# Optimization experiments

Hardware: AMD Instinct MI355X
Metric: run time of the kernel (lower is better)

The kernel has to match this reference:

```python
import jax, jax.numpy as jnp
from jax import lax
import numpy as np

K_SIZE = 3  # SteerableKernelBase.create_radial(3)


def _radial_basis_3x3():
    """Orthonormal radial steerable basis on a 3x3 grid.
    Returns 6 unit-norm kernels: [k0_center, k0_ring, k1_cos, k1_sin, k2_cos, k2_sin]."""
    ys, xs = np.mgrid[-1:2, -1:2].astype(np.float32)
    ang = np.arctan2(ys, xs)
    ring = (np.hypot(xs, ys) > 0).astype(np.float32)

    def unit(k):
        return (k / np.linalg.norm(k)).astype(np.float32)

    b0c = np.zeros((3, 3), np.float32); b0c[1, 1] = 1.0
    basis = np.stack([
        b0c,                       # k=0, r=0
        unit(ring),                # k=0, r=1
        unit(np.cos(ang) * ring),  # k=1 real
        unit(np.sin(ang) * ring),  # k=1 imag
        unit(np.cos(2 * ang) * ring),  # k=2 real
        unit(np.sin(2 * ang) * ring),  # k=2 imag
    ])
    return jnp.asarray(basis)  # (6, 3, 3)


def setup_inputs() -> dict:
    key = jax.random.key(0)
    k1, k2, k3 = jax.random.split(key, 3)
    N, C_in, C_out, H, W = 16, 64, 64, 128, 128
    x = jax.random.normal(k1, (N, C_in, H, W), dtype=jnp.float32)
    # steering angle field in [0,1); alpha = (cos 2*pi*theta, sin 2*pi*theta) is unitary
    theta = jax.random.uniform(k2, (N, 1, H, W), dtype=jnp.float32)
    # steerable weights: (n_out, n_in, 4) -> [k0 center, k0 ring, k1, k2]
    fan_in = C_in * K_SIZE * K_SIZE
    std = jnp.sqrt(2.0 / fan_in)  # relu gain init as in steerable_base.init_weights
    weights = jax.random.normal(k3, (C_out, C_in, 4), dtype=jnp.float32) * std
    bias = jnp.zeros((C_out,), dtype=jnp.float32)
    return {"x": x, "theta": theta, "weights": weights, "bias": bias}


def reference(x, theta, weights, bias):
    basis = _radial_basis_3x3()  # (6,3,3)
    O = weights.shape[0]
    w = weights[..., None, None]  # (O,I,4,1,1)
    # Synthesize per-harmonic kernels (O,I,3,3) from the steerable basis
    k0 = w[:, :, 0] * basis[0] + w[:, :, 1] * basis[1]
    k1r = w[:, :, 2] * basis[2]
    k1i = w[:, :, 2] * basis[3]
    k2r = w[:, :, 3] * basis[4]
    k2i = w[:, :, 3] * basis[5]
    ker = jnp.concatenate([k0, k1r, k1i, k2r, k2i], axis=0)  # (5O, I, 3, 3)

    z = lax.conv_general_dilated(
        x, ker, window_strides=(1, 1), padding="SAME",
        dimension_numbers=("NCHW", "OIHW", "NCHW"))  # (N, 5O, H, W)
    N, _, H, W = z.shape
    z = z.reshape(N, 5, O, H, W)

    # angle harmonics cos(k*alpha), sin(k*alpha); alpha unitary so rho=1 path
    a = 2.0 * jnp.pi * theta  # (N,1,H,W)
    c1, s1 = jnp.cos(a), jnp.sin(a)
    c2 = 2.0 * c1 * c1 - 1.0
    s2 = 2.0 * s1 * c1

    out = (z[:, 0] + c1 * z[:, 1] + s1 * z[:, 2]
           + c2 * z[:, 3] + s2 * z[:, 4])
    return out + bias[None, :, None, None]
```

## Files before the change

kernel.cpp:

```cpp
#include <hip/hip_runtime.h>


typedef __bf16 bf16x8 __attribute__((ext_vector_type(8)));
typedef float  f32x16 __attribute__((ext_vector_type(16)));
typedef float  f32x4  __attribute__((ext_vector_type(4)));
typedef unsigned int u32;
typedef const __attribute__((address_space(1))) u32* gp_t;
typedef __attribute__((address_space(3))) u32* lp_t;

#define HH 128
#define WW 128
#define CHCH 8
#define NCHUNK 8
#define NBUF 3
#define RROWS 10
#define RCOLS 40
#define CHF 400
#define CHIMG 65536

__global__ void wt_repack(const float* __restrict__ wt,
                          unsigned short* __restrict__ wb) {
    int i = blockIdx.x * 256 + threadIdx.x;
    int o = i >> 8, k = i & 255;
    union { float f; u32 u; } v; v.f = wt[i];
    unsigned short b = (unsigned short)((v.u + 0x7FFF + ((v.u >> 16) & 1)) >> 16);
    int kcg = k >> 4, hxx = (k >> 3) & 1, r = k & 7;
    wb[((kcg * 2 + hxx) * 64 + o) * 8 + r] = b;
}

__global__ __launch_bounds__(256, 4) void steered_conv_mfma(
    const float* __restrict__ x, const float* __restrict__ theta,
    const unsigned short* __restrict__ wb, const float* __restrict__ bias,
    float* __restrict__ out)
{
    __shared__ __attribute__((aligned(16))) float lds[NBUF][CHCH][CHF];

    const int tid = threadIdx.x;
    const int wid = tid >> 6, lane = tid & 63;
    const int pc = lane & 31, hx = lane >> 5;

    const int bb = blockIdx.x;
    const int swz = (bb & 7) * 128 + (bb >> 3);
    const int n = swz >> 6;
    const int ty = (swz >> 2) & 15, tx = swz & 3;
    const int h0 = ty * 8, w0 = tx * 32;
    const int p0 = wid * 2;

    const int oA = lane * 16;
    const int rA = oA / 160;
    const int cA = oA - rA * 160;
    int ghA = h0 - 1 + rA; ghA = ghA < 0 ? 0 : (ghA > 127 ? 127 : ghA);
    int srcA = ghA * 512 + w0 * 4 - 16 + cA;
    srcA = srcA < 0 ? 0 : srcA;
    const bool skA = (w0 == 0 && cA < 16) || (w0 == 96 && cA >= 144)
                   || (h0 == 0 && rA == 0);

    const int oB = 1024 + lane * 16;
    const int rB = oB / 160;
    const int cB = oB - rB * 160;
    int ghB = h0 - 1 + rB; ghB = ghB < 0 ? 0 : (ghB > 127 ? 127 : ghB);
    int srcB = ghB * 512 + w0 * 4 - 16 + cB;
    srcB = srcB < 0 ? 0 : (srcB > CHIMG - 16 ? CHIMG - 16 : srcB);
    const bool skB = (lane >= 36) || (w0 == 0 && cB < 16) || (w0 == 96 && cB >= 144)
                   || (h0 == 120 && rB == 9);

    const char* xn = (const char*)x + (size_t)n * 64 * CHIMG;

    float s1a, c1a, s1b, c1b;
    __sincosf(6.2831853071795864769f * theta[(n*HH + h0+p0)*WW + w0+pc], &s1a, &c1a);
    __sincosf(6.2831853071795864769f * theta[(n*HH + h0+p0+1)*WW + w0+pc], &s1b, &c1b);
    const float c2a = 2.f*c1a*c1a - 1.f, s2a = 2.f*s1a*c1a;
    const float c2b = 2.f*c1b*c1b - 1.f, s2b = 2.f*s1b*c1b;

    if ((h0 == 0) | (h0 == 120) | (w0 == 0) | (w0 == 96)) {
        f32x4* z = (f32x4*)&lds[0][0][0];
        for (int i = tid; i < NBUF * CHCH * CHF / 4; i += 256)
            z[i] = f32x4{0.f, 0.f, 0.f, 0.f};
    }
    __syncthreads();

    auto stage = [&](int t) {
        const char* xc = xn + (size_t)(t * CHCH) * CHIMG;
        #pragma unroll
        for (int j = 0; j < 2; ++j) {
            const int ch = wid * 2 + j;
            const char* s = xc + ch * CHIMG;
            char* d = (char*)&lds[t % NBUF][ch][0];
            if (!skA) __builtin_amdgcn_global_load_lds((gp_t)(s + srcA), (lp_t)d, 16, 0, 0);
            if (!skB) __builtin_amdgcn_global_load_lds((gp_t)(s + srcB), (lp_t)(d + 1024), 16, 0, 0);
        }
    };

    stage(0);
    stage(1);

    f32x16 acc00, acc01, acc10, acc11;
    #pragma unroll
    for (int r = 0; r < 16; ++r) { acc00[r]=0.f; acc01[r]=0.f; acc10[r]=0.f; acc11[r]=0.f; }

    const float RS  = 0.35355339059327373f;
    const float HMR = 0.14644660940672627f;
    const unsigned short* wbl = wb + (hx * 64 + pc) * 8;

    #pragma unroll
    for (int c = 0; c < NCHUNK; ++c) {
        asm volatile("s_waitcnt vmcnt(4)" ::: "memory");
        const unsigned short* wr0 = wbl + c * 2048;
        const bf16x8 A00 = *(const bf16x8*)(wr0);
        const bf16x8 A01 = *(const bf16x8*)(wr0 + 256);
        const bf16x8 A10 = *(const bf16x8*)(wr0 + 1024);
        const bf16x8 A11 = *(const bf16x8*)(wr0 + 1280);
        __builtin_amdgcn_sched_barrier(0);
        __builtin_amdgcn_s_barrier();
        if (c < NCHUNK - 2) stage(c + 2);
        __builtin_amdgcn_sched_barrier(0);

        const float* tb = &lds[c % NBUF][0][p0 * RCOLS + pc + 3];
        #pragma unroll
        for (int kc = 0; kc < 2; ++kc) {
            bf16x8 b0, b1;
            #pragma unroll
            for (int cs = 0; cs < 2; ++cs) {
                const float* t = tb + (kc * 4 + hx * 2 + cs) * CHF;
                const float t00=t[0],   t01=t[1],   t02=t[2];
                const float t10=t[40],  t11=t[41],  t12=t[42];
                const float t20=t[80],  t21=t[81],  t22=t[82];
                const float t30=t[120], t31=t[121], t32=t[122];
                const float S0=t00+t01+t02, S1=t10+t11+t12;
                const float S2=t20+t21+t22, S3=t30+t31+t32;
                const float D0=t02-t00, D1=t12-t10, D2=t22-t20, D3=t32-t30;
                {
                    const float F1 = RS * (S0 + S2 + S1 - t11);
                    const float B2 = RS * (D0 + D2) + 0.5f * D1;
                    const float B3 = RS * (S2 - S0) + HMR * (t21 - t01);
                    const float B4 = 0.5f * (S1 - t11 - t01 - t21);
                    const float B5 = 0.5f * (D2 - D0);
                    b0[cs*4+0] = (__bf16)t11;
                    b0[cs*4+1] = (__bf16)F1;
                    b0[cs*4+2] = (__bf16)(c1a * B2 + s1a * B3);
                    b0[cs*4+3] = (__bf16)(c2a * B4 + s2a * B5);
                }
                {
                    const float F1 = RS * (S1 + S3 + S2 - t21);
                    const float B2 = RS * (D1 + D3) + 0.5f * D2;
                    const float B3 = RS * (S3 - S1) + HMR * (t31 - t11);
                    const float B4 = 0.5f * (S2 - t21 - t11 - t31);
                    const float B5 = 0.5f * (D3 - D1);
                    b1[cs*4+0] = (__bf16)t21;
                    b1[cs*4+1] = (__bf16)F1;
                    b1[cs*4+2] = (__bf16)(c1b * B2 + s1b * B3);
                    b1[cs*4+3] = (__bf16)(c2b * B4 + s2b * B5);
                }
            }
            const bf16x8 A0 = kc ? A10 : A00;
            const bf16x8 A1 = kc ? A11 : A01;
            __builtin_amdgcn_s_setprio(1);
            acc00 = __builtin_amdgcn_mfma_f32_32x32x16_bf16(A0, b0, acc00, 0, 0, 0);
            acc01 = __builtin_amdgcn_mfma_f32_32x32x16_bf16(A1, b0, acc01, 0, 0, 0);
            acc10 = __builtin_amdgcn_mfma_f32_32x32x16_bf16(A0, b1, acc10, 0, 0, 0);
            acc11 = __builtin_amdgcn_mfma_f32_32x32x16_bf16(A1, b1, acc11, 0, 0, 0);
            __builtin_amdgcn_s_setprio(0);
        }
    }

    const size_t hw = (size_t)HH * WW;
    float* op = out + (size_t)n * 64 * hw + (size_t)(h0 + p0) * WW + w0 + pc;
    #pragma unroll
    for (int r = 0; r < 16; ++r) {
        const int o = (r & 3) + 8 * (r >> 2) + 4 * hx;
        const float bo = bias[o], bo2 = bias[o + 32];
        op[(size_t)o * hw]             = acc00[r] + bo;
        op[(size_t)(o + 32) * hw]      = acc01[r] + bo2;
        op[(size_t)o * hw + WW]        = acc10[r] + bo;
        op[(size_t)(o + 32) * hw + WW] = acc11[r] + bo2;
    }
}

extern "C" void kernel_launch(void* const* d_in, const int* in_sizes, int n_in,
                              void* d_out, int out_size, void* d_ws, size_t ws_size,
                              hipStream_t stream) {
    const float* x     = (const float*)d_in[0];
    const float* theta = (const float*)d_in[1];
    const float* wt    = (const float*)d_in[2];
    const float* bias  = (const float*)d_in[3];
    float* out = (float*)d_out;
    unsigned short* wb = (unsigned short*)d_ws;

    wt_repack<<<64, 256, 0, stream>>>(wt, wb);

    steered_conv_mfma<<<1024, 256, 0, stream>>>(x, theta, wb, bias, out);
}
```

Baseline: 41.91 us.

## Use full-width 1024-thread tiles with LDS-resident weights and double-buffered input rows

Blocks now cover a full 128-column, 8-row strip with 16 waves instead of a 32-column tile with 4 waves. This removes the horizontal halo duplication; left and right borders are handled by clamped indices and multiplication by 0/1 masks. The whole bf16 weight matrix is loaded once into LDS per block instead of being read from global memory each chunk. Input staging drops from triple to double buffering with a full vmcnt(0) wait every chunk, which may expose more load latency. The larger LDS footprint and 1024-thread blocks also cut occupancy, and only 256 blocks are launched.

```diff
diff --git a/kernel.cpp b/kernel.cpp
--- a/kernel.cpp
+++ b/kernel.cpp
@@ -3,19 +3,13 @@
 
 typedef __bf16 bf16x8 __attribute__((ext_vector_type(8)));
 typedef float  f32x16 __attribute__((ext_vector_type(16)));
-typedef float  f32x4  __attribute__((ext_vector_type(4)));
 typedef unsigned int u32;
 typedef const __attribute__((address_space(1))) u32* gp_t;
 typedef __attribute__((address_space(3))) u32* lp_t;
 
 #define HH 128
 #define WW 128
-#define CHCH 8
-#define NCHUNK 8
-#define NBUF 3
-#define RROWS 10
-#define RCOLS 40
-#define CHF 400
+#define HW 16384
 #define CHIMG 65536
 
 __global__ void wt_repack(const float* __restrict__ wt,
@@ -28,71 +22,84 @@
     wb[((kcg * 2 + hxx) * 64 + o) * 8 + r] = b;
 }
 
-__global__ __launch_bounds__(256, 4) void steered_conv_mfma(
+__global__ __launch_bounds__(1024, 4) void steered_conv_mfma(
     const float* __restrict__ x, const float* __restrict__ theta,
     const unsigned short* __restrict__ wb, const float* __restrict__ bias,
     float* __restrict__ out)
 {
-    __shared__ __attribute__((aligned(16))) float lds[NBUF][CHCH][CHF];
+    __shared__ unsigned short wlds[16384];
+    __shared__ __attribute__((aligned(16))) float xb[2][8][12][128];
 
-    const int tid = threadIdx.x;
-    const int wid = tid >> 6, lane = tid & 63;
-    const int pc = lane & 31, hx = lane >> 5;
+    const int tid  = threadIdx.x;
+    const int W    = tid >> 6, lane = tid & 63;
+    const int pc   = lane & 31, hx = lane >> 5;
+    const int p0   = (W >> 2) * 2;
+    const int w    = (W & 3) * 32 + pc;
 
-    const int bb = blockIdx.x;
-    const int swz = (bb & 7) * 128 + (bb >> 3);
-    const int n = swz >> 6;
-    const int ty = (swz >> 2) & 15, tx = swz & 3;
-    const int h0 = ty * 8, w0 = tx * 32;
-    const int p0 = wid * 2;
-
-    const int oA = lane * 16;
-    const int rA = oA / 160;
-    const int cA = oA - rA * 160;
-    int ghA = h0 - 1 + rA; ghA = ghA < 0 ? 0 : (ghA > 127 ? 127 : ghA);
-    int srcA = ghA * 512 + w0 * 4 - 16 + cA;
-    srcA = srcA < 0 ? 0 : srcA;
-    const bool skA = (w0 == 0 && cA < 16) || (w0 == 96 && cA >= 144)
-                   || (h0 == 0 && rA == 0);
-
-    const int oB = 1024 + lane * 16;
-    const int rB = oB / 160;
-    const int cB = oB - rB * 160;
-    int ghB = h0 - 1 + rB; ghB = ghB < 0 ? 0 : (ghB > 127 ? 127 : ghB);
-    int srcB = ghB * 512 + w0 * 4 - 16 + cB;
-    srcB = srcB < 0 ? 0 : (srcB > CHIMG - 16 ? CHIMG - 16 : srcB);
-    const bool skB = (lane >= 36) || (w0 == 0 && cB < 16) || (w0 == 96 && cB >= 144)
-                   || (h0 == 120 && rB == 9);
+    const int bb  = blockIdx.x;
+    const int swz = (bb & 7) * 32 + (bb >> 3);
+    const int n   = swz >> 4;
+    const int h0  = (swz & 15) * 8;
 
     const char* xn = (const char*)x + (size_t)n * 64 * CHIMG;
 
+    {
+        const char* s = (const char*)wb + tid * 16;
+        char* d = (char*)wlds + W * 1024;
+        __builtin_amdgcn_global_load_lds((gp_t)s, (lp_t)d, 16, 0, 0);
+        __builtin_amdgcn_global_load_lds((gp_t)(s + 16384), (lp_t)(d + 16384), 16, 0, 0);
+    }
+
+    const int i0  = W * 3;
+    const int ch0 = i0 / 6,       pr0 = i0 - ch0 * 6;
+    const int ch1 = (i0+1) / 6,   pr1 = (i0+1) - ch1 * 6;
+    const int ch2 = (i0+2) / 6,   pr2 = (i0+2) - ch2 * 6;
+    char* const xldsb = (char*)&xb[0][0][0][0];
+
+    auto stage = [&](int t) {
+        const char* xc = xn + (size_t)(t * 8) * CHIMG + lane * 16;
+        char* db = xldsb + (t & 1) * 49152;
+        if (!((h0 == 0 && pr0 == 0) || (h0 == 120 && pr0 == 5)))
+            __builtin_amdgcn_global_load_lds(
+                (gp_t)(xc + ch0 * CHIMG + (h0 - 2 + 2 * pr0) * 512),
+                (lp_t)(db + ch0 * 6144 + pr0 * 1024), 16, 0, 0);
+        if (!((h0 == 0 && pr1 == 0) || (h0 == 120 && pr1 == 5)))
+            __builtin_amdgcn_global_load_lds(
+                (gp_t)(xc + ch1 * CHIMG + (h0 - 2 + 2 * pr1) * 512),
+                (lp_t)(db + ch1 * 6144 + pr1 * 1024), 16, 0, 0);
+        if (!((h0 == 0 && pr2 == 0) || (h0 == 120 && pr2 == 5)))
+            __builtin_amdgcn_global_load_lds(
+                (gp_t)(xc + ch2 * CHIMG + (h0 - 2 + 2 * pr2) * 512),
+                (lp_t)(db + ch2 * 6144 + pr2 * 1024), 16, 0, 0);
+    };
+    stage(0);
+
     float s1a, c1a, s1b, c1b;
-    __sincosf(6.2831853071795864769f * theta[(n*HH + h0+p0)*WW + w0+pc], &s1a, &c1a);
-    __sincosf(6.2831853071795864769f * theta[(n*HH + h0+p0+1)*WW + w0+pc], &s1b, &c1b);
+    __sincosf(6.2831853071795864769f * theta[(n*HH + h0+p0)*WW + w], &s1a, &c1a);
+    __sincosf(6.2831853071795864769f * theta[(n*HH + h0+p0+1)*WW + w], &s1b, &c1b);
     const float c2a = 2.f*c1a*c1a - 1.f, s2a = 2.f*s1a*c1a;
     const float c2b = 2.f*c1b*c1b - 1.f, s2b = 2.f*s1b*c1b;
 
-    if ((h0 == 0) | (h0 == 120) | (w0 == 0) | (w0 == 96)) {
-        f32x4* z = (f32x4*)&lds[0][0][0];
-        for (int i = tid; i < NBUF * CHCH * CHF / 4; i += 256)
-            z[i] = f32x4{0.f, 0.f, 0.f, 0.f};
+    if (h0 == 0 || h0 == 120) {
+        const int sb = (h0 == 0) ? 0 : 10;
+        for (int i = tid; i < 4096; i += 1024) {
+            const int b   = i >> 11;
+            const int ch  = (i >> 8) & 7;
+            const int rr  = (i >> 7) & 1;
+            const int col = i & 127;
+            xb[b][ch][sb + rr][col] = 0.f;
+        }
     }
     __syncthreads();
 
-    auto stage = [&](int t) {
-        const char* xc = xn + (size_t)(t * CHCH) * CHIMG;
-        #pragma unroll
-        for (int j = 0; j < 2; ++j) {
-            const int ch = wid * 2 + j;
-            const char* s = xc + ch * CHIMG;
-            char* d = (char*)&lds[t % NBUF][ch][0];
-            if (!skA) __builtin_amdgcn_global_load_lds((gp_t)(s + srcA), (lp_t)d, 16, 0, 0);
-            if (!skB) __builtin_amdgcn_global_load_lds((gp_t)(s + srcB), (lp_t)(d + 1024), 16, 0, 0);
-        }
-    };
+    const float fL = (w > 0) ? 1.f : 0.f;
+    const float fR = (w < WW - 1) ? 1.f : 0.f;
+    const int  wLo = (w > 0) ? w - 1 : 0;
+    const int  wRo = (w < WW - 1) ? w + 1 : WW - 1;
 
-    stage(0);
-    stage(1);
+    const float* pL = &xb[0][0][0][0] + hx * 3072 + (p0 + 1) * 128 + wLo;
+    const float* pC = &xb[0][0][0][0] + hx * 3072 + (p0 + 1) * 128 + w;
+    const float* pR = &xb[0][0][0][0] + hx * 3072 + (p0 + 1) * 128 + wRo;
 
     f32x16 acc00, acc01, acc10, acc11;
     #pragma unroll
@@ -100,60 +107,60 @@
 
     const float RS  = 0.35355339059327373f;
     const float HMR = 0.14644660940672627f;
-    const unsigned short* wbl = wb + (hx * 64 + pc) * 8;
 
     #pragma unroll
-    for (int c = 0; c < NCHUNK; ++c) {
-        asm volatile("s_waitcnt vmcnt(4)" ::: "memory");
-        const unsigned short* wr0 = wbl + c * 2048;
-        const bf16x8 A00 = *(const bf16x8*)(wr0);
-        const bf16x8 A01 = *(const bf16x8*)(wr0 + 256);
-        const bf16x8 A10 = *(const bf16x8*)(wr0 + 1024);
-        const bf16x8 A11 = *(const bf16x8*)(wr0 + 1280);
+    for (int c = 0; c < 8; ++c) {
+        asm volatile("s_waitcnt vmcnt(0)" ::: "memory");
+        __builtin_amdgcn_s_barrier();
         __builtin_amdgcn_sched_barrier(0);
-        __builtin_amdgcn_s_barrier();
-        if (c < NCHUNK - 2) stage(c + 2);
+        if (c < 7) stage(c + 1);
         __builtin_amdgcn_sched_barrier(0);
 
-        const float* tb = &lds[c % NBUF][0][p0 * RCOLS + pc + 3];
         #pragma unroll
         for (int kc = 0; kc < 2; ++kc) {
+            const int kcg = c * 2 + kc;
+            const bf16x8 A0 = *(const bf16x8*)&wlds[((kcg*2 + hx)*64 + pc) * 8];
+            const bf16x8 A1 = *(const bf16x8*)&wlds[((kcg*2 + hx)*64 + 32 + pc) * 8];
             bf16x8 b0, b1;
             #pragma unroll
             for (int cs = 0; cs < 2; ++cs) {
-                const float* t = tb + (kc * 4 + hx * 2 + cs) * CHF;
-                const float t00=t[0],   t01=t[1],   t02=t[2];
-                const float t10=t[40],  t11=t[41],  t12=t[42];
-                const float t20=t[80],  t21=t[81],  t22=t[82];
-                const float t30=t[120], t31=t[121], t32=t[122];
-                const float S0=t00+t01+t02, S1=t10+t11+t12;
-                const float S2=t20+t21+t22, S3=t30+t31+t32;
-                const float D0=t02-t00, D1=t12-t10, D2=t22-t20, D3=t32-t30;
+                const int off = (c & 1) * 12288 + (kc * 4 + cs) * 1536;
+                float S[4], D[4], C[4];
+                #pragma unroll
+                for (int r = 0; r < 4; ++r) {
+                    const float tL = pL[off + r * 128];
+                    const float tC = pC[off + r * 128];
+                    const float tR = pR[off + r * 128];
+                    const float a = fL * tL, cc = fR * tR;
+                    S[r] = a + tC + cc;
+                    D[r] = cc - a;
+                    C[r] = tC;
+                }
                 {
-                    const float F1 = RS * (S0 + S2 + S1 - t11);
-                    const float B2 = RS * (D0 + D2) + 0.5f * D1;
-                    const float B3 = RS * (S2 - S0) + HMR * (t21 - t01);
-                    const float B4 = 0.5f * (S1 - t11 - t01 - t21);
-                    const float B5 = 0.5f * (D2 - D0);
-                    b0[cs*4+0] = (__bf16)t11;
+                    const float T  = S[1] - C[1];
+                    const float F1 = RS * (S[0] + S[2] + T);
+                    const float B2 = RS * (D[0] + D[2]) + 0.5f * D[1];
+                    const float B3 = RS * (S[2] - S[0]) + HMR * (C[2] - C[0]);
+                    const float B4 = 0.5f * (T - (C[0] + C[2]));
+                    const float B5 = 0.5f * (D[2] - D[0]);
+                    b0[cs*4+0] = (__bf16)C[1];
                     b0[cs*4+1] = (__bf16)F1;
                     b0[cs*4+2] = (__bf16)(c1a * B2 + s1a * B3);
                     b0[cs*4+3] = (__bf16)(c2a * B4 + s2a * B5);
                 }
                 {
-                    const float F1 = RS * (S1 + S3 + S2 - t21);
-                    const float B2 = RS * (D1 + D3) + 0.5f * D2;
-                    const float B3 = RS * (S3 - S1) + HMR * (t31 - t11);
-                    const float B4 = 0.5f * (S2 - t21 - t11 - t31);
-                    const float B5 = 0.5f * (D3 - D1);
-                    b1[cs*4+0] = (__bf16)t21;
+                    const float T  = S[2] - C[2];
+                    const float F1 = RS * (S[1] + S[3] + T);
+                    const float B2 = RS * (D[1] + D[3]) + 0.5f * D[2];
+                    const float B3 = RS * (S[3] - S[1]) + HMR * (C[3] - C[1]);
+                    const float B4 = 0.5f * (T - (C[1] + C[3]));
+                    const float B5 = 0.5f * (D[3] - D[1]);
+                    b1[cs*4+0] = (__bf16)C[2];
                     b1[cs*4+1] = (__bf16)F1;
                     b1[cs*4+2] = (__bf16)(c1b * B2 + s1b * B3);
                     b1[cs*4+3] = (__bf16)(c2b * B4 + s2b * B5);
                 }
             }
-            const bf16x8 A0 = kc ? A10 : A00;
-            const bf16x8 A1 = kc ? A11 : A01;
             __builtin_amdgcn_s_setprio(1);
             acc00 = __builtin_amdgcn_mfma_f32_32x32x16_bf16(A0, b0, acc00, 0, 0, 0);
             acc01 = __builtin_amdgcn_mfma_f32_32x32x16_bf16(A1, b0, acc01, 0, 0, 0);
@@ -163,8 +170,8 @@
         }
     }
 
-    const size_t hw = (size_t)HH * WW;
-    float* op = out + (size_t)n * 64 * hw + (size_t)(h0 + p0) * WW + w0 + pc;
+    const size_t hw = (size_t)HW;
+    float* op = out + (size_t)n * 64 * hw + (size_t)(h0 + p0) * WW + w;
     #pragma unroll
     for (int r = 0; r < 16; ++r) {
         const int o = (r & 3) + 8 * (r >> 2) + 4 * hx;
@@ -188,5 +195,5 @@
 
     wt_repack<<<64, 256, 0, stream>>>(wt, wb);
 
-    steered_conv_mfma<<<1024, 256, 0, stream>>>(x, theta, wb, bias, out);
+    steered_conv_mfma<<<256, 1024, 0, stream>>>(x, theta, wb, bias, out);
 }
```

Result: slower. 57.23 us (+36.5%).

## Prefetch weight fragments one chunk ahead with double-buffered registers

Applied to the files above, without the earlier changes.

Weight A-operand loads for the next channel chunk are issued a chunk early into alternating even/odd register sets, so the MFMA loop no longer waits on global weight loads issued at the top of the same iteration. The vmcnt accounting is adjusted to drain all loads on the last chunk. Launch bounds drop from 4 to 3 waves-per-EU occupancy hint to give room for the extra 32 VGPRs of prefetched weights. This trades occupancy for latency hiding; the vmcnt(4) count may now be inconsistent with the extra in-flight weight loads mixed with LDS DMA loads.

```diff
diff --git a/kernel.cpp b/kernel.cpp
--- a/kernel.cpp
+++ b/kernel.cpp
@@ -28,7 +28,7 @@
     wb[((kcg * 2 + hxx) * 64 + o) * 8 + r] = b;
 }
 
-__global__ __launch_bounds__(256, 4) void steered_conv_mfma(
+__global__ __launch_bounds__(256, 3) void steered_conv_mfma(
     const float* __restrict__ x, const float* __restrict__ theta,
     const unsigned short* __restrict__ wb, const float* __restrict__ bias,
     float* __restrict__ out)
@@ -91,7 +91,17 @@
         }
     };
 
+    const unsigned short* wbl = wb + (hx * 64 + pc) * 8;
+    bf16x8 wE0, wE1, wE2, wE3, wO0, wO1, wO2, wO3;
+
     stage(0);
+    {
+        const unsigned short* wr = wbl;
+        wE0 = *(const bf16x8*)(wr);
+        wE1 = *(const bf16x8*)(wr + 256);
+        wE2 = *(const bf16x8*)(wr + 1024);
+        wE3 = *(const bf16x8*)(wr + 1280);
+    }
     stage(1);
 
     f32x16 acc00, acc01, acc10, acc11;
@@ -100,20 +110,34 @@
 
     const float RS  = 0.35355339059327373f;
     const float HMR = 0.14644660940672627f;
-    const unsigned short* wbl = wb + (hx * 64 + pc) * 8;
 
     #pragma unroll
     for (int c = 0; c < NCHUNK; ++c) {
-        asm volatile("s_waitcnt vmcnt(4)" ::: "memory");
-        const unsigned short* wr0 = wbl + c * 2048;
-        const bf16x8 A00 = *(const bf16x8*)(wr0);
-        const bf16x8 A01 = *(const bf16x8*)(wr0 + 256);
-        const bf16x8 A10 = *(const bf16x8*)(wr0 + 1024);
-        const bf16x8 A11 = *(const bf16x8*)(wr0 + 1280);
+        if (c == NCHUNK - 1) asm volatile("s_waitcnt vmcnt(0)" ::: "memory");
+        else                 asm volatile("s_waitcnt vmcnt(4)" ::: "memory");
         __builtin_amdgcn_sched_barrier(0);
         __builtin_amdgcn_s_barrier();
-        if (c < NCHUNK - 2) stage(c + 2);
+        if (c + 1 < NCHUNK) {
+            const unsigned short* wr = wbl + (c + 1) * 2048;
+            if ((c + 1) & 1) {
+                wO0 = *(const bf16x8*)(wr);
+                wO1 = *(const bf16x8*)(wr + 256);
+                wO2 = *(const bf16x8*)(wr + 1024);
+                wO3 = *(const bf16x8*)(wr + 1280);
+            } else {
+                wE0 = *(const bf16x8*)(wr);
+                wE1 = *(const bf16x8*)(wr + 256);
+                wE2 = *(const bf16x8*)(wr + 1024);
+                wE3 = *(const bf16x8*)(wr + 1280);
+            }
+        }
+        if (c + 2 < NCHUNK) stage(c + 2);
         __builtin_amdgcn_sched_barrier(0);
+
+        const bf16x8 A00 = (c & 1) ? wO0 : wE0;
+        const bf16x8 A01 = (c & 1) ? wO1 : wE1;
+        const bf16x8 A10 = (c & 1) ? wO2 : wE2;
+        const bf16x8 A11 = (c & 1) ? wO3 : wE3;
 
         const float* tb = &lds[c % NBUF][0][p0 * RCOLS + pc + 3];
         #pragma unroll
```

Result: no change. 41.84 us (-0.2%).

## Use 512-thread blocks with one output row per wave and LDS-staged weights

Applied to the files above, without the earlier changes.

Doubles the block to 8 waves so each wave computes a single output row with two accumulators, where previously each wave did two rows with four. The repacked bf16 weights are staged once per block into LDS with async global-to-LDS loads, replacing per-chunk global loads. Each stage now has one wave per input channel, and explicit left/right edge masks are added to the 3x3 stencil math. The intent is more waves to hide latency and cheaper weight access. In exchange, each output row now reads and reduces its own three input rows, losing the row reuse the two-row scheme had, and LDS use grows to roughly 70 KB per block, which limits how many blocks fit per CU.

```diff
diff --git a/kernel.cpp b/kernel.cpp
--- a/kernel.cpp
+++ b/kernel.cpp
@@ -10,12 +10,9 @@
 
 #define HH 128
 #define WW 128
-#define CHCH 8
+#define HW 16384
 #define NCHUNK 8
 #define NBUF 3
-#define RROWS 10
-#define RCOLS 40
-#define CHF 400
 #define CHIMG 65536
 
 __global__ void wt_repack(const float* __restrict__ wt,
@@ -28,15 +25,16 @@
     wb[((kcg * 2 + hxx) * 64 + o) * 8 + r] = b;
 }
 
-__global__ __launch_bounds__(256, 4) void steered_conv_mfma(
+__global__ __launch_bounds__(512, 4) void steered_conv_mfma(
     const float* __restrict__ x, const float* __restrict__ theta,
     const unsigned short* __restrict__ wb, const float* __restrict__ bias,
     float* __restrict__ out)
 {
-    __shared__ __attribute__((aligned(16))) float lds[NBUF][CHCH][CHF];
+    __shared__ unsigned short wlds[16384];
+    __shared__ __attribute__((aligned(16))) float xs[NBUF][8][400];
 
     const int tid = threadIdx.x;
-    const int wid = tid >> 6, lane = tid & 63;
+    const int W = tid >> 6, lane = tid & 63;
     const int pc = lane & 31, hx = lane >> 5;
 
     const int bb = blockIdx.x;
@@ -44,7 +42,12 @@
     const int n = swz >> 6;
     const int ty = (swz >> 2) & 15, tx = swz & 3;
     const int h0 = ty * 8, w0 = tx * 32;
-    const int p0 = wid * 2;
+    const int hr = h0 + W;
+    const int w  = w0 + pc;
+
+    float s1, c1;
+    __sincosf(6.2831853071795864769f * theta[(n * HH + hr) * WW + w], &s1, &c1);
+    const float c2 = 2.f * c1 * c1 - 1.f, s2 = 2.f * s1 * c1;
 
     const int oA = lane * 16;
     const int rA = oA / 160;
@@ -66,113 +69,95 @@
 
     const char* xn = (const char*)x + (size_t)n * 64 * CHIMG;
 
-    float s1a, c1a, s1b, c1b;
-    __sincosf(6.2831853071795864769f * theta[(n*HH + h0+p0)*WW + w0+pc], &s1a, &c1a);
-    __sincosf(6.2831853071795864769f * theta[(n*HH + h0+p0+1)*WW + w0+pc], &s1b, &c1b);
-    const float c2a = 2.f*c1a*c1a - 1.f, s2a = 2.f*s1a*c1a;
-    const float c2b = 2.f*c1b*c1b - 1.f, s2b = 2.f*s1b*c1b;
-
     if ((h0 == 0) | (h0 == 120) | (w0 == 0) | (w0 == 96)) {
-        f32x4* z = (f32x4*)&lds[0][0][0];
-        for (int i = tid; i < NBUF * CHCH * CHF / 4; i += 256)
+        f32x4* z = (f32x4*)&xs[0][0][0];
+        for (int i = tid; i < NBUF * 8 * 100; i += 512)
             z[i] = f32x4{0.f, 0.f, 0.f, 0.f};
     }
     __syncthreads();
 
+    {
+        const char* s = (const char*)wb + W * 1024 + lane * 16;
+        char* d = (char*)wlds + W * 1024;
+        #pragma unroll
+        for (int r = 0; r < 4; ++r)
+            __builtin_amdgcn_global_load_lds((gp_t)(s + r * 8192),
+                                             (lp_t)(d + r * 8192), 16, 0, 0);
+    }
+
     auto stage = [&](int t) {
-        const char* xc = xn + (size_t)(t * CHCH) * CHIMG;
-        #pragma unroll
-        for (int j = 0; j < 2; ++j) {
-            const int ch = wid * 2 + j;
-            const char* s = xc + ch * CHIMG;
-            char* d = (char*)&lds[t % NBUF][ch][0];
-            if (!skA) __builtin_amdgcn_global_load_lds((gp_t)(s + srcA), (lp_t)d, 16, 0, 0);
-            if (!skB) __builtin_amdgcn_global_load_lds((gp_t)(s + srcB), (lp_t)(d + 1024), 16, 0, 0);
-        }
+        const char* s = xn + (size_t)(t * 8 + W) * CHIMG;
+        char* d = (char*)&xs[t % NBUF][W][0];
+        if (!skA) __builtin_amdgcn_global_load_lds((gp_t)(s + srcA), (lp_t)d, 16, 0, 0);
+        if (!skB) __builtin_amdgcn_global_load_lds((gp_t)(s + srcB), (lp_t)(d + 1024), 16, 0, 0);
     };
-
     stage(0);
     stage(1);
 
-    f32x16 acc00, acc01, acc10, acc11;
+    f32x16 acc0, acc1;
     #pragma unroll
-    for (int r = 0; r < 16; ++r) { acc00[r]=0.f; acc01[r]=0.f; acc10[r]=0.f; acc11[r]=0.f; }
+    for (int r = 0; r < 16; ++r) { acc0[r] = 0.f; acc1[r] = 0.f; }
 
     const float RS  = 0.35355339059327373f;
     const float HMR = 0.14644660940672627f;
-    const unsigned short* wbl = wb + (hx * 64 + pc) * 8;
+    const float fL  = (w > 0) ? 1.f : 0.f;
+    const float fR  = (w < WW - 1) ? 1.f : 0.f;
 
     #pragma unroll
     for (int c = 0; c < NCHUNK; ++c) {
-        asm volatile("s_waitcnt vmcnt(4)" ::: "memory");
-        const unsigned short* wr0 = wbl + c * 2048;
-        const bf16x8 A00 = *(const bf16x8*)(wr0);
-        const bf16x8 A01 = *(const bf16x8*)(wr0 + 256);
-        const bf16x8 A10 = *(const bf16x8*)(wr0 + 1024);
-        const bf16x8 A11 = *(const bf16x8*)(wr0 + 1280);
+        if (c == NCHUNK - 1) asm volatile("s_waitcnt vmcnt(0)" ::: "memory");
+        else                 asm volatile("s_waitcnt vmcnt(2)" ::: "memory");
         __builtin_amdgcn_sched_barrier(0);
         __builtin_amdgcn_s_barrier();
-        if (c < NCHUNK - 2) stage(c + 2);
+        if (c + 2 < NCHUNK) stage(c + 2);
         __builtin_amdgcn_sched_barrier(0);
 
-        const float* tb = &lds[c % NBUF][0][p0 * RCOLS + pc + 3];
         #pragma unroll
         for (int kc = 0; kc < 2; ++kc) {
-            bf16x8 b0, b1;
+            const int kcg = c * 2 + kc;
+            bf16x8 b;
             #pragma unroll
             for (int cs = 0; cs < 2; ++cs) {
-                const float* t = tb + (kc * 4 + hx * 2 + cs) * CHF;
-                const float t00=t[0],   t01=t[1],   t02=t[2];
-                const float t10=t[40],  t11=t[41],  t12=t[42];
-                const float t20=t[80],  t21=t[81],  t22=t[82];
-                const float t30=t[120], t31=t[121], t32=t[122];
-                const float S0=t00+t01+t02, S1=t10+t11+t12;
-                const float S2=t20+t21+t22, S3=t30+t31+t32;
-                const float D0=t02-t00, D1=t12-t10, D2=t22-t20, D3=t32-t30;
-                {
-                    const float F1 = RS * (S0 + S2 + S1 - t11);
-                    const float B2 = RS * (D0 + D2) + 0.5f * D1;
-                    const float B3 = RS * (S2 - S0) + HMR * (t21 - t01);
-                    const float B4 = 0.5f * (S1 - t11 - t01 - t21);
-                    const float B5 = 0.5f * (D2 - D0);
-                    b0[cs*4+0] = (__bf16)t11;
-                    b0[cs*4+1] = (__bf16)F1;
-                    b0[cs*4+2] = (__bf16)(c1a * B2 + s1a * B3);
-                    b0[cs*4+3] = (__bf16)(c2a * B4 + s2a * B5);
+                const float* p = &xs[c % NBUF][0][0]
+                               + (kc * 4 + hx * 2 + cs) * 400 + W * 40 + pc + 4;
+                float S[3], D[3], C[3];
+                #pragma unroll
+                for (int rr = 0; rr < 3; ++rr) {
+                    const float tL = p[rr * 40 - 1];
+                    const float tC = p[rr * 40];
+                    const float tR = p[rr * 40 + 1];
+                    const float a = fL * tL, cc = fR * tR;
+                    S[rr] = a + tC + cc;
+                    D[rr] = cc - a;
+                    C[rr] = tC;
                 }
-                {
-                    const float F1 = RS * (S1 + S3 + S2 - t21);
-                    const float B2 = RS * (D1 + D3) + 0.5f * D2;
-                    const float B3 = RS * (S3 - S1) + HMR * (t31 - t11);
-                    const float B4 = 0.5f * (S2 - t21 - t11 - t31);
-                    const float B5 = 0.5f * (D3 - D1);
-                    b1[cs*4+0] = (__bf16)t21;
-                    b1[cs*4+1] = (__bf16)F1;
-                    b1[cs*4+2] = (__bf16)(c1b * B2 + s1b * B3);
-                    b1[cs*4+3] = (__bf16)(c2b * B4 + s2b * B5);
-                }
+                const float T  = S[1] - C[1];
+                const float F1 = RS * (S[0] + S[2] + T);
+                const float B2 = RS * (D[0] + D[2]) + 0.5f * D[1];
+                const float B3 = RS * (S[2] - S[0]) + HMR * (C[2] - C[0]);
+                const float B4 = 0.5f * (T - (C[0] + C[2]));
+                const float B5 = 0.5f * (D[2] - D[0]);
+                b[cs*4+0] = (__bf16)C[1];
+                b[cs*4+1] = (__bf16)F1;
+                b[cs*4+2] = (__bf16)(c1 * B2 + s1 * B3);
+                b[cs*4+3] = (__bf16)(c2 * B4 + s2 * B5);
             }
-            const bf16x8 A0 = kc ? A10 : A00;
-            const bf16x8 A1 = kc ? A11 : A01;
+            const bf16x8 A0 = *(const bf16x8*)&wlds[((kcg*2 + hx)*64 + pc) * 8];
+            const bf16x8 A1 = *(const bf16x8*)&wlds[((kcg*2 + hx)*64 + 32 + pc) * 8];
             __builtin_amdgcn_s_setprio(1);
-            acc00 = __builtin_amdgcn_mfma_f32_32x32x16_bf16(A0, b0, acc00, 0, 0, 0);
-            acc01 = __builtin_amdgcn_mfma_f32_32x32x16_bf16(A1, b0, acc01, 0, 0, 0);
-            acc10 = __builtin_amdgcn_mfma_f32_32x32x16_bf16(A0, b1, acc10, 0, 0, 0);
-            acc11 = __builtin_amdgcn_mfma_f32_32x32x16_bf16(A1, b1, acc11, 0, 0, 0);
+            acc0 = __builtin_amdgcn_mfma_f32_32x32x16_bf16(A0, b, acc0, 0, 0, 0);
+            acc1 = __builtin_amdgcn_mfma_f32_32x32x16_bf16(A1, b, acc1, 0, 0, 0);
             __builtin_amdgcn_s_setprio(0);
         }
     }
 
-    const size_t hw = (size_t)HH * WW;
-    float* op = out + (size_t)n * 64 * hw + (size_t)(h0 + p0) * WW + w0 + pc;
+    const size_t hw = (size_t)HW;
+    float* op = out + (size_t)n * 64 * hw + (size_t)hr * WW + w;
     #pragma unroll
     for (int r = 0; r < 16; ++r) {
         const int o = (r & 3) + 8 * (r >> 2) + 4 * hx;
-        const float bo = bias[o], bo2 = bias[o + 32];
-        op[(size_t)o * hw]             = acc00[r] + bo;
-        op[(size_t)(o + 32) * hw]      = acc01[r] + bo2;
-        op[(size_t)o * hw + WW]        = acc10[r] + bo;
-        op[(size_t)(o + 32) * hw + WW] = acc11[r] + bo2;
+        op[(size_t)o * hw]        = acc0[r] + bias[o];
+        op[(size_t)(o + 32) * hw] = acc1[r] + bias[o + 32];
     }
 }
 
@@ -188,5 +173,5 @@
 
     wt_repack<<<64, 256, 0, stream>>>(wt, wb);
 
-    steered_conv_mfma<<<1024, 256, 0, stream>>>(x, theta, wb, bias, out);
+    steered_conv_mfma<<<1024, 512, 0, stream>>>(x, theta, wb, bias, out);
 }
```

After: 52.22 us. +24.6%, slower.
